# Kernel tuning notes

Hardware: AMD Instinct MI355X
Metric: run time of the kernel (lower is better)

Reference implementation:

```python
import jax, jax.numpy as jnp
import numpy as np

DIM = 128
WINDOW_TOKENS = 64  # window_size**2 = 8*8


def _conv3x3(x, w):
    # x: [B,C,H,W], w: [O,I,3,3], padding=1 (SAME)
    return jax.lax.conv_general_dilated(
        x, w, window_strides=(1, 1), padding='SAME',
        dimension_numbers=('NCHW', 'OIHW', 'NCHW'))


def _pixel_shuffle2(x):
    # torch.nn.PixelShuffle(2): [B, C*4, H, W] -> [B, C, 2H, 2W]
    B, C4, H, W = x.shape
    C = C4 // 4
    x = x.reshape(B, C, 2, 2, H, W)
    x = x.transpose(0, 1, 4, 2, 5, 3)  # [B, C, H, 2, W, 2]
    return x.reshape(B, C, H * 2, W * 2)


def setup_inputs() -> dict:
    key = jax.random.key(0)
    ks = jax.random.split(key, 12)
    B, C = 4, DIM
    f0 = jax.random.normal(ks[0], (B, C, 64, 64), jnp.float32)
    f1 = jax.random.normal(ks[1], (B, C, 128, 128), jnp.float32)
    f2 = jax.random.normal(ks[2], (B, C, 256, 256), jnp.float32)
    s = 0.02
    # Linear weights stored as [in, out] so forward is x @ W
    Wq = jax.random.normal(ks[3], (C, C), jnp.float32) * s
    Wk = jax.random.normal(ks[4], (C, C), jnp.float32) * s
    Wv = jax.random.normal(ks[5], (C, C), jnp.float32) * s
    Wql = jax.random.normal(ks[6], (C, C), jnp.float32) * s
    Wkl = jax.random.normal(ks[7], (C, C), jnp.float32) * s
    Wvl = jax.random.normal(ks[8], (C, C), jnp.float32) * s
    gate_w = jax.random.normal(ks[9], (2 * C, C), jnp.float32) * s
    conv0 = jax.random.normal(ks[10], (4 * C, C, 3, 3), jnp.float32) * s
    conv1 = jax.random.normal(ks[11], (4 * C, C, 3, 3), jnp.float32) * s
    return dict(f0=f0, f1=f1, f2=f2, Wq=Wq, Wk=Wk, Wv=Wv,
                Wql=Wql, Wkl=Wkl, Wvl=Wvl, gate_w=gate_w,
                conv0=conv0, conv1=conv1)


def reference(f0, f1, f2, Wq, Wk, Wv, Wql, Wkl, Wvl, gate_w, conv0, conv1):
    feats = (f0, f1, f2)
    B, C = f0.shape[0], f0.shape[1]
    scale = C ** (-0.5)
    # flatten+concat: [B, N, C]
    toks = [f.reshape(B, C, -1).transpose(0, 2, 1) for f in feats]
    x = jnp.concatenate(toks, axis=1)
    N = x.shape[1]
    wt = WINDOW_TOKENS
    nw = N // wt  # N is divisible by wt for these shapes (no padding)
    windows = x.reshape(B, nw, wt, C)

    # ---- global path (mode='center'): attention over window means ----
    centers = windows.mean(axis=2)  # [B, nw, C]
    Q = centers @ Wq
    K = centers @ Wk
    V = centers @ Wv
    attn = jax.nn.softmax(jnp.einsum('bnc,bmc->bnm', Q, K) * scale, axis=-1)
    y_centers = jnp.einsum('bnm,bmc->bnc', attn, V) * centers
    y_global = jnp.broadcast_to(y_centers[:, :, None, :], (B, nw, wt, C)).reshape(B, N, C)

    # ---- local path: attention within each window (batched over windows) ----
    Ql = windows @ Wql
    Kl = windows @ Wkl
    Vl = windows @ Wvl
    attn_l = jax.nn.softmax(jnp.einsum('bwqc,bwkc->bwqk', Ql, Kl) * scale, axis=-1)
    y_local = (jnp.einsum('bwqk,bwkc->bwqc', attn_l, Vl) * windows).reshape(B, N, C)

    # ---- gated fusion ----
    alpha = jax.nn.sigmoid(jnp.concatenate([y_global, y_local], axis=-1) @ gate_w)
    y = alpha * y_global + (1.0 - alpha) * y_local

    # ---- reshape back to feature maps ----
    maps = []
    start = 0
    for f in feats:
        H, W = f.shape[2], f.shape[3]
        cnt = H * W
        maps.append(y[:, start:start + cnt, :].transpose(0, 2, 1).reshape(B, C, H, W))
        start += cnt
    # ---- inverse wavelet reconstruction (conv3x3 -> pixel shuffle -> add) ----
    outputs = [maps[0]]
    z = maps[0]
    z = _pixel_shuffle2(_conv3x3(z, conv0)) + maps[1]
    outputs.append(z)
    z = _pixel_shuffle2(_conv3x3(z, conv1)) + maps[2]
    outputs.append(z)
    return tuple(outputs)
```

## Files before the change

### kernel.cpp

```cpp
#include <hip/hip_runtime.h>
#include <math.h>

#define WT 64
#define NWIN 1344
#define NP 1408
constexpr float SCALE = 0.088388347648318447f;

#define OUT0 0
#define OUT1 2097152
#define OUT2 10485760

typedef __attribute__((ext_vector_type(8))) short bfrag;
typedef __attribute__((ext_vector_type(8))) _Float16 hfrag;
typedef __attribute__((ext_vector_type(4))) float f32x4;

#define MFMA16 __builtin_amdgcn_mfma_f32_16x16x32_bf16
#define MFMA16H __builtin_amdgcn_mfma_f32_16x16x32_f16

__device__ __forceinline__ unsigned short f2b(float f) {
    union { float f; unsigned u; } v; v.f = f;
    unsigned r = v.u + 0x7fffu + ((v.u >> 16) & 1u);
    return (unsigned short)(r >> 16);
}
__device__ __forceinline__ float b2f(unsigned short u) {
    union { unsigned u; float f; } v; v.u = ((unsigned)u) << 16; return v.f;
}
__device__ __forceinline__ int pack2(float a, float b) {
    return (int)f2b(a) | ((int)f2b(b) << 16);
}

__device__ __forceinline__ bfrag ld256(const char* region, int row, int k) {
    int off = (2 * k) ^ ((row & 7) << 4);
    return *(const bfrag*)(region + row * 256 + off);
}
__device__ __forceinline__ bfrag ld128(const char* region, int row, int k) {
    int off = (2 * k) ^ ((row & 7) << 4);
    return *(const bfrag*)(region + row * 128 + off);
}

__global__ void k_mm(const float* __restrict__ Wq, const float* __restrict__ Wk,
                     float* __restrict__ Mglob) {
    int i = blockIdx.x, j = threadIdx.x;
    float acc = 0.f;
    for (int k = 0; k < 128; ++k) acc += Wq[i * 128 + k] * Wk[j * 128 + k];
    Mglob[i * 128 + j] = acc;
}

__global__ void k_prep(const float* __restrict__ Wql, const float* __restrict__ Wkl,
                       const float* __restrict__ Wvl, const float* __restrict__ gw,
                       unsigned short* __restrict__ MtB,
                       unsigned short* __restrict__ WvltB,
                       unsigned short* __restrict__ G1tB,
                       unsigned short* __restrict__ G0tB) {
    int n = blockIdx.x, k = threadIdx.x;
    if (blockIdx.y == 0) {
        float a = 0.f;
        for (int c = 0; c < 128; ++c) a += Wkl[n * 128 + c] * Wql[k * 128 + c];
        MtB[n * 128 + k] = f2b(a);
    } else if (blockIdx.y == 1) {
        WvltB[n * 128 + k] = f2b(Wvl[k * 128 + n]);
    } else if (blockIdx.y == 2) {
        G1tB[n * 128 + k] = f2b(gw[(128 + k) * 128 + n]);
    } else {
        G0tB[n * 128 + k] = f2b(gw[k * 128 + n]);
    }
}

__global__ __launch_bounds__(256) void k_prep_conv(
    const float* __restrict__ w0, const float* __restrict__ w1,
    _Float16* __restrict__ W0, _Float16* __restrict__ W1) {
    int idx = blockIdx.x * 256 + threadIdx.x;
    const float* w = blockIdx.y ? w1 : w0;
    _Float16* o = blockIdx.y ? W1 : W0;
    int slice = idx >> 14, rem = idx & 16383;
    int oc = rem >> 5, k = rem & 31;
    int ics = slice / 9, tap = slice - ics * 9;
    o[idx] = (_Float16)w[((size_t)oc * 128 + ics * 32 + k) * 9 + tap];
}

__device__ __forceinline__ void window_src(int n0, const float* f0, const float* f1,
                                           const float* f2, const float*& f, int& p0,
                                           int& HW, int& obase) {
    if (n0 < 4096)        { f = f0; p0 = n0;          HW = 4096;  obase = OUT0; }
    else if (n0 < 20480)  { f = f1; p0 = n0 - 4096;   HW = 16384; obase = OUT1; }
    else                  { f = f2; p0 = n0 - 20480;  HW = 65536; obase = OUT2; }
}

__global__ __launch_bounds__(256) void k_centers(
    const float* __restrict__ f0, const float* __restrict__ f1,
    const float* __restrict__ f2, float* __restrict__ ctr,
    unsigned short* __restrict__ ctrb) {
    int w = blockIdx.x, b = blockIdx.y;
    const float* f; int p0, HW, ob;
    window_src(w * WT, f0, f1, f2, f, p0, HW, ob);
    int lane = threadIdx.x & 63, cg = threadIdx.x >> 6;
    for (int c = cg; c < 128; c += 4) {
        float v = f[(b * 128 + c) * HW + p0 + lane];
        #pragma unroll
        for (int off = 32; off; off >>= 1) v += __shfl_xor(v, off);
        if (lane == 0) {
            float mv = v * (1.0f / 64.0f);
            ctr[(b * NWIN + w) * 128 + c] = mv;
            ctrb[(b * NWIN + w) * 128 + c] = f2b(mv);
        }
    }
}

__global__ __launch_bounds__(128) void k_tgvg(
    const float* __restrict__ ctr, const float* __restrict__ Mglob,
    const float* __restrict__ Wv, unsigned short* __restrict__ Tgb,
    unsigned short* __restrict__ Vgt) {
    int n = blockIdx.x, b = blockIdx.y;
    int row = b * NWIN + n;
    int c = threadIdx.x;
    __shared__ __align__(16) float crow[128];
    crow[c] = ctr[row * 128 + c];
    __syncthreads();
    float a1 = 0.f, a2 = 0.f;
    for (int k = 0; k < 128; ++k) {
        float cv = crow[k];
        a1 += cv * Mglob[k * 128 + c];
        a2 += cv * Wv[k * 128 + c];
    }
    Tgb[row * 128 + c] = f2b(a1);
    Vgt[((size_t)b * 128 + c) * NP + n] = f2b(a2);
}

__global__ __launch_bounds__(256, 1) void k_qk(
    const unsigned short* __restrict__ Tgb, const unsigned short* __restrict__ ctrb,
    unsigned short* __restrict__ P) {
    extern __shared__ unsigned short Srow[];
    __shared__ float mxs[32], invs[32];
    int blk = blockIdx.x, b = blockIdx.y;
    int mb = blk * 32;
    int tid = threadIdx.x, wid = tid >> 6, lane = tid & 63;
    int lr = lane & 15, lg = lane >> 4;
    int wm = (wid & 1) * 16, wn = (wid >> 1) * 32;

    const unsigned short* Arow = Tgb + ((size_t)b * NWIN + mb + wm + lr) * 128;
    for (int tile = 0; tile < 21; ++tile) {
        int nb = tile * 64 + wn;
        f32x4 acc[2] = {};
        #pragma unroll
        for (int ks = 0; ks < 4; ++ks) {
            int k = ks * 32 + lg * 8;
            bfrag a = *(const bfrag*)(Arow + k);
            #pragma unroll
            for (int nt = 0; nt < 2; ++nt) {
                bfrag bb = *(const bfrag*)(ctrb + ((size_t)b * NWIN + nb + nt * 16 + lr) * 128 + k);
                acc[nt] = MFMA16(a, bb, acc[nt], 0, 0, 0);
            }
        }
        #pragma unroll
        for (int nt = 0; nt < 2; ++nt) {
            int col = nb + nt * 16 + lr;
            #pragma unroll
            for (int r = 0; r < 4; ++r) {
                int mrow = wm + 4 * lg + r;
                Srow[mrow * 1344 + col] = f2b(acc[nt][r]);
            }
        }
    }
    __syncthreads();
    {
        int row = tid >> 3, sub = tid & 7;
        const unsigned short* sr = Srow + row * 1344;
        float mx = -1e30f;
        for (int c = sub; c < 1344; c += 8) mx = fmaxf(mx, b2f(sr[c]));
        mx = fmaxf(mx, __shfl_xor(mx, 1));
        mx = fmaxf(mx, __shfl_xor(mx, 2));
        mx = fmaxf(mx, __shfl_xor(mx, 4));
        float sum = 0.f;
        for (int c = sub; c < 1344; c += 8) sum += __expf((b2f(sr[c]) - mx) * SCALE);
        sum += __shfl_xor(sum, 1);
        sum += __shfl_xor(sum, 2);
        sum += __shfl_xor(sum, 4);
        if (sub == 0) { mxs[row] = mx; invs[row] = 1.0f / sum; }
    }
    __syncthreads();
    unsigned short* Pb = P + ((size_t)b * NWIN + mb) * NP;
    for (int idx = tid; idx < 32 * (NP / 8); idx += 256) {
        int row = idx / (NP / 8), c8 = idx % (NP / 8);
        float mx = mxs[row], inv = invs[row];
        unsigned short o[8];
        #pragma unroll
        for (int e = 0; e < 8; ++e) {
            int c = c8 * 8 + e;
            float p = (c < 1344) ? __expf((b2f(Srow[row * 1344 + c]) - mx) * SCALE) * inv : 0.f;
            o[e] = f2b(p);
        }
        *(int4*)(Pb + row * NP + c8 * 8) = *(int4*)o;
    }
}

__global__ __launch_bounds__(256) void k_pv(
    const unsigned short* __restrict__ P, const unsigned short* __restrict__ Vgt,
    const float* __restrict__ ctr, float* __restrict__ ycen,
    unsigned short* __restrict__ ycenb) {
    int blk = blockIdx.x, b = blockIdx.y;
    int mb = blk * 32;
    int tid = threadIdx.x, wid = tid >> 6, lane = tid & 63;
    int lr = lane & 15, lg = lane >> 4;
    int cb = wid * 32;
    f32x4 acc[2][2] = {};
    const unsigned short* Pb = P + ((size_t)b * NWIN + mb) * NP;
    const unsigned short* Vb = Vgt + (size_t)b * 128 * NP;
    for (int it = 0; it < 44; ++it) {
        int k = it * 32 + lg * 8;
        bfrag a0 = *(const bfrag*)(Vb + (size_t)(cb + lr) * NP + k);
        bfrag a1 = *(const bfrag*)(Vb + (size_t)(cb + 16 + lr) * NP + k);
        bfrag b0 = *(const bfrag*)(Pb + (size_t)lr * NP + k);
        bfrag b1 = *(const bfrag*)(Pb + (size_t)(16 + lr) * NP + k);
        acc[0][0] = MFMA16(a0, b0, acc[0][0], 0, 0, 0);
        acc[0][1] = MFMA16(a0, b1, acc[0][1], 0, 0, 0);
        acc[1][0] = MFMA16(a1, b0, acc[1][0], 0, 0, 0);
        acc[1][1] = MFMA16(a1, b1, acc[1][1], 0, 0, 0);
    }
    #pragma unroll
    for (int ci = 0; ci < 2; ++ci)
        #pragma unroll
        for (int mj = 0; mj < 2; ++mj) {
            int c0 = cb + ci * 16 + 4 * lg;
            int m = mb + mj * 16 + lr;
            size_t base = ((size_t)b * NWIN + m) * 128 + c0;
            float4 cv = *(const float4*)(ctr + base);
            float4 y;
            y.x = acc[ci][mj][0] * cv.x;
            y.y = acc[ci][mj][1] * cv.y;
            y.z = acc[ci][mj][2] * cv.z;
            y.w = acc[ci][mj][3] * cv.w;
            *(float4*)(ycen + base) = y;
            int2 pv; pv.x = pack2(y.x, y.y); pv.y = pack2(y.z, y.w);
            *(int2*)(ycenb + base) = pv;
        }
}

__global__ __launch_bounds__(256) void k_g0(
    const unsigned short* __restrict__ ycenb, const unsigned short* __restrict__ G0tB,
    float* __restrict__ g0g) {
    int blk = blockIdx.x, b = blockIdx.y;
    int mb = blk * 32;
    int tid = threadIdx.x, wid = tid >> 6, lane = tid & 63;
    int lr = lane & 15, lg = lane >> 4;
    int nb = wid * 32;
    f32x4 acc[2][2] = {};
    const unsigned short* Yb = ycenb + ((size_t)b * NWIN + mb) * 128;
    #pragma unroll
    for (int ks = 0; ks < 4; ++ks) {
        int k = ks * 32 + lg * 8;
        bfrag a0 = *(const bfrag*)(G0tB + (nb + lr) * 128 + k);
        bfrag a1 = *(const bfrag*)(G0tB + (nb + 16 + lr) * 128 + k);
        bfrag b0 = *(const bfrag*)(Yb + lr * 128 + k);
        bfrag b1 = *(const bfrag*)(Yb + (16 + lr) * 128 + k);
        acc[0][0] = MFMA16(a0, b0, acc[0][0], 0, 0, 0);
        acc[0][1] = MFMA16(a0, b1, acc[0][1], 0, 0, 0);
        acc[1][0] = MFMA16(a1, b0, acc[1][0], 0, 0, 0);
        acc[1][1] = MFMA16(a1, b1, acc[1][1], 0, 0, 0);
    }
    #pragma unroll
    for (int ni = 0; ni < 2; ++ni)
        #pragma unroll
        for (int mj = 0; mj < 2; ++mj) {
            int m = mb + mj * 16 + lr;
            int n0 = nb + ni * 16 + 4 * lg;
            #pragma unroll
            for (int r = 0; r < 4; ++r)
                g0g[((size_t)b * NWIN + m) * 128 + n0 + r] = acc[ni][mj][r];
        }
}

#define XB_OFF 0
#define WT_OFF 16384
#define XM_OFF 49152
#define VT_OFF 65536
#define SMEM_SZ 81920

__global__ __launch_bounds__(256, 2) void k_local_mfma(
    const float* __restrict__ f0, const float* __restrict__ f1,
    const float* __restrict__ f2,
    const unsigned short* __restrict__ MtB,
    const unsigned short* __restrict__ WvltB,
    const unsigned short* __restrict__ G1tB,
    const float* __restrict__ g0g, const float* __restrict__ ycen,
    float* __restrict__ out) {
    extern __shared__ char smem[];
    char* Xb = smem + XB_OFF;
    char* Wt = smem + WT_OFF;
    char* XMb = smem + XM_OFF;
    char* Vt = smem + VT_OFF;

    int w = blockIdx.x, b = blockIdx.y;
    const float* f; int p0, HW, obase;
    window_src(w * WT, f0, f1, f2, f, p0, HW, obase);

    int tid = threadIdx.x;
    int wid = tid >> 6, lane = tid & 63;
    int lr = lane & 15, lg = lane >> 4;

    {
        int t0 = tid & 63, cq = tid >> 6;
        const float* src = f + (size_t)(b * 128 + cq * 32) * HW + p0 + t0;
        float xv[32];
        #pragma unroll
        for (int i = 0; i < 32; ++i) xv[i] = src[(size_t)i * HW];
        int4 wreg[8];
        const int4* wsrc = (const int4*)MtB;
        #pragma unroll
        for (int j = 0; j < 8; ++j) wreg[j] = wsrc[j * 256 + tid];
        #pragma unroll
        for (int j = 0; j < 4; ++j) {
            int c0 = cq * 32 + j * 8;
            int4 v;
            v.x = pack2(xv[j * 8 + 0], xv[j * 8 + 1]);
            v.y = pack2(xv[j * 8 + 2], xv[j * 8 + 3]);
            v.z = pack2(xv[j * 8 + 4], xv[j * 8 + 5]);
            v.w = pack2(xv[j * 8 + 6], xv[j * 8 + 7]);
            *(int4*)(Xb + t0 * 256 + ((2 * c0) ^ ((t0 & 7) << 4))) = v;
        }
        #pragma unroll
        for (int j = 0; j < 8; ++j) {
            int ci = j * 256 + tid, n = ci >> 4, pos = ci & 15;
            *(int4*)(Wt + n * 256 + ((pos * 16) ^ ((n & 7) << 4))) = wreg[j];
        }
    }
    __syncthreads();

    int t = 16 * wid + lr;

    {
        f32x4 acc[8] = {};
        #pragma unroll
        for (int ks = 0; ks < 4; ++ks) {
            int k = ks * 32 + lg * 8;
            bfrag xb = ld256(Xb, t, k);
            #pragma unroll
            for (int ct = 0; ct < 8; ++ct) {
                bfrag am = ld256(Wt, 16 * ct + lr, k);
                acc[ct] = MFMA16(am, xb, acc[ct], 0, 0, 0);
            }
        }
        #pragma unroll
        for (int ct = 0; ct < 8; ++ct) {
            int c0 = 16 * ct + 4 * lg;
            int2 v; v.x = pack2(acc[ct][0], acc[ct][1]); v.y = pack2(acc[ct][2], acc[ct][3]);
            *(int2*)(XMb + t * 256 + ((2 * c0) ^ ((t & 7) << 4))) = v;
        }
    }
    __syncthreads();

    {
        int4 wreg[8];
        const int4* wsrc = (const int4*)WvltB;
        #pragma unroll
        for (int j = 0; j < 8; ++j) wreg[j] = wsrc[j * 256 + tid];

        f32x4 s[4] = {};
        #pragma unroll
        for (int ks = 0; ks < 4; ++ks) {
            int k = ks * 32 + lg * 8;
            bfrag bxm = ld256(XMb, t, k);
            #pragma unroll
            for (int ut = 0; ut < 4; ++ut) {
                bfrag ax = ld256(Xb, 16 * ut + lr, k);
                s[ut] = MFMA16(ax, bxm, s[ut], 0, 0, 0);
            }
        }
        float m = -1e30f;
        #pragma unroll
        for (int ut = 0; ut < 4; ++ut)
            #pragma unroll
            for (int r = 0; r < 4; ++r) m = fmaxf(m, s[ut][r]);
        m = fmaxf(m, __shfl_xor(m, 16));
        m = fmaxf(m, __shfl_xor(m, 32));
        float sum = 0.f;
        float e[4][4];
        #pragma unroll
        for (int ut = 0; ut < 4; ++ut)
            #pragma unroll
            for (int r = 0; r < 4; ++r) {
                e[ut][r] = __expf((s[ut][r] - m) * SCALE);
                sum += e[ut][r];
            }
        sum += __shfl_xor(sum, 16);
        sum += __shfl_xor(sum, 32);
        float pinv = 1.0f / sum;
        __syncthreads();
        #pragma unroll
        for (int ut = 0; ut < 4; ++ut) {
            int u0 = 16 * ut + 4 * lg;
            int2 v;
            v.x = pack2(e[ut][0] * pinv, e[ut][1] * pinv);
            v.y = pack2(e[ut][2] * pinv, e[ut][3] * pinv);
            *(int2*)(XMb + t * 128 + ((2 * u0) ^ ((t & 7) << 4))) = v;
        }
        #pragma unroll
        for (int j = 0; j < 8; ++j) {
            int ci = j * 256 + tid, n = ci >> 4, pos = ci & 15;
            *(int4*)(Wt + n * 256 + ((pos * 16) ^ ((n & 7) << 4))) = wreg[j];
        }
    }
    __syncthreads();

    int4 wregG[8];
    {
        const int4* wsrc = (const int4*)G1tB;
        #pragma unroll
        for (int j = 0; j < 8; ++j) wregG[j] = wsrc[j * 256 + tid];

        f32x4 vacc[8] = {};
        #pragma unroll
        for (int ks = 0; ks < 4; ++ks) {
            int k = ks * 32 + lg * 8;
            bfrag ax = ld256(Xb, t, k);
            #pragma unroll
            for (int ct = 0; ct < 8; ++ct) {
                bfrag bw = ld256(Wt, 16 * ct + lr, k);
                vacc[ct] = MFMA16(ax, bw, vacc[ct], 0, 0, 0);
            }
        }
        #pragma unroll
        for (int ct = 0; ct < 8; ++ct) {
            int c = 16 * ct + lr;
            int u0 = 16 * wid + 4 * lg;
            int2 v; v.x = pack2(vacc[ct][0], vacc[ct][1]); v.y = pack2(vacc[ct][2], vacc[ct][3]);
            *(int2*)(Vt + c * 128 + ((2 * u0) ^ ((c & 7) << 4))) = v;
        }
    }
    __syncthreads();

    float yl[8][4];
    float4 yg4[8], g04[8];
    {
        #pragma unroll
        for (int j = 0; j < 8; ++j) {
            int ci = j * 256 + tid, n = ci >> 4, pos = ci & 15;
            *(int4*)(Wt + n * 256 + ((pos * 16) ^ ((n & 7) << 4))) = wregG[j];
        }
        size_t rbase = ((size_t)b * NWIN + w) * 128 + 4 * lg;
        #pragma unroll
        for (int nt = 0; nt < 8; ++nt) {
            yg4[nt] = *(const float4*)(ycen + rbase + 16 * nt);
            g04[nt] = *(const float4*)(g0g + rbase + 16 * nt);
        }
        f32x4 y[8] = {};
        #pragma unroll
        for (int us = 0; us < 2; ++us) {
            int u = us * 32 + lg * 8;
            bfrag bp = ld128(XMb, t, u);
            #pragma unroll
            for (int ct = 0; ct < 8; ++ct) {
                bfrag av = ld128(Vt, 16 * ct + lr, u);
                y[ct] = MFMA16(av, bp, y[ct], 0, 0, 0);
            }
        }
        #pragma unroll
        for (int ct = 0; ct < 8; ++ct) {
            int c0 = 16 * ct + 4 * lg;
            int2 xw = *(const int2*)(Xb + t * 256 + ((2 * c0) ^ ((t & 7) << 4)));
            float x0 = b2f((unsigned short)(xw.x & 0xffff));
            float x1 = b2f((unsigned short)((unsigned)xw.x >> 16));
            float x2 = b2f((unsigned short)(xw.y & 0xffff));
            float x3 = b2f((unsigned short)((unsigned)xw.y >> 16));
            yl[ct][0] = y[ct][0] * x0;
            yl[ct][1] = y[ct][1] * x1;
            yl[ct][2] = y[ct][2] * x2;
            yl[ct][3] = y[ct][3] * x3;
            int2 v; v.x = pack2(yl[ct][0], yl[ct][1]); v.y = pack2(yl[ct][2], yl[ct][3]);
            *(int2*)(Xb + t * 256 + ((2 * c0) ^ ((t & 7) << 4))) = v;
        }
    }
    __syncthreads();

    {
        f32x4 g[8] = {};
        #pragma unroll
        for (int ks = 0; ks < 4; ++ks) {
            int k = ks * 32 + lg * 8;
            bfrag byl = ld256(Xb, t, k);
            #pragma unroll
            for (int nt = 0; nt < 8; ++nt) {
                bfrag ag = ld256(Wt, 16 * nt + lr, k);
                g[nt] = MFMA16(ag, byl, g[nt], 0, 0, 0);
            }
        }
        #pragma unroll
        for (int nt = 0; nt < 8; ++nt) {
            float gv[4] = {g04[nt].x, g04[nt].y, g04[nt].z, g04[nt].w};
            float yv4[4] = {yg4[nt].x, yg4[nt].y, yg4[nt].z, yg4[nt].w};
            #pragma unroll
            for (int r = 0; r < 4; ++r) {
                int c = 16 * nt + 4 * lg + r;
                float a = 1.0f / (1.0f + __expf(-(g[nt][r] + gv[r])));
                float yv = a * yv4[r] + (1.0f - a) * yl[nt][r];
                out[obase + (size_t)(b * 128 + c) * HW + p0 + t] = yv;
            }
        }
    }
}

template <int H, int W>
__global__ __launch_bounds__(256, 2) void k_conv_mfma(
    const float* __restrict__ in, const _Float16* __restrict__ Wcv,
    float* __restrict__ out) {
    constexpr int TXN = W / 32;
    int tile = blockIdx.x;
    int ty = tile / TXN, tx = tile % TXN;
    int y0 = ty * 4, x0 = tx * 32;
    int ob = blockIdx.y * 256;
    int b = blockIdx.z;

    __shared__ __align__(16) char sXs[16384];

    int tid = threadIdx.x;
    int wid = tid >> 6, lane = tid & 63;
    int lr = lane & 15, lg = lane >> 4;

    f32x4 acc[8][4] = {};

    int sy = tid / 34, sx = tid - sy * 34;
    int gy = y0 + sy - 1, gx = x0 + sx - 1;
    bool act = tid < 204;
    bool ok = act && gy >= 0 && gy < H && gx >= 0 && gx < W;
    const float* gp = in + (size_t)b * 128 * H * W + (size_t)gy * W + gx;
    int xswz = (tid >> 3) & 1;

    const _Float16* wbase = Wcv + (size_t)(ob + lr) * 32 + lg * 8;

    hfrag afC[4], afN[4];
    #pragma unroll
    for (int n = 0; n < 4; ++n)
        afC[n] = *(const hfrag*)(wbase + (size_t)(wid * 4 + n) * 512);

    if (act) {
        float xv[32];
        if (ok) {
            #pragma unroll
            for (int ic = 0; ic < 32; ++ic) xv[ic] = gp[(size_t)ic * H * W];
        } else {
            #pragma unroll
            for (int ic = 0; ic < 32; ++ic) xv[ic] = 0.f;
        }
        #pragma unroll
        for (int s = 0; s < 4; ++s) {
            _Float16 hh[8];
            #pragma unroll
            for (int e = 0; e < 8; ++e) hh[e] = (_Float16)xv[s * 8 + e];
            *(int4*)(sXs + tid * 80 + ((s ^ xswz) << 4)) = *(int4*)hh;
        }
    }
    __syncthreads();

    for (int ics = 0; ics < 4; ++ics) {
        if (ics) {
            __syncthreads();
            if (act) {
                float xv[32];
                if (ok) {
                    #pragma unroll
                    for (int ic = 0; ic < 32; ++ic)
                        xv[ic] = gp[(size_t)(ics * 32 + ic) * H * W];
                } else {
                    #pragma unroll
                    for (int ic = 0; ic < 32; ++ic) xv[ic] = 0.f;
                }
                #pragma unroll
                for (int s = 0; s < 4; ++s) {
                    _Float16 hh[8];
                    #pragma unroll
                    for (int e = 0; e < 8; ++e) hh[e] = (_Float16)xv[s * 8 + e];
                    *(int4*)(sXs + tid * 80 + ((s ^ xswz) << 4)) = *(int4*)hh;
                }
            }
            __syncthreads();
        }
        #pragma unroll
        for (int tap = 0; tap < 9; ++tap) {
            int kg = ics * 9 + tap;
            if (tap < 8 || ics < 3) {
                const _Float16* ws = wbase + (size_t)(kg + 1) * 16384;
                #pragma unroll
                for (int n = 0; n < 4; ++n)
                    afN[n] = *(const hfrag*)(ws + (size_t)(wid * 4 + n) * 512);
            }
            int dy = tap / 3, dx = tap - dy * 3;
            hfrag bf[8];
            #pragma unroll
            for (int m = 0; m < 8; ++m) {
                int row = ((m >> 1) + dy) * 34 + (m & 1) * 16 + lr + dx;
                bf[m] = *(const hfrag*)(sXs + row * 80 + ((lg ^ ((row >> 3) & 1)) << 4));
            }
            #pragma unroll
            for (int m = 0; m < 8; ++m)
                #pragma unroll
                for (int n = 0; n < 4; ++n)
                    acc[m][n] = MFMA16H(afC[n], bf[m], acc[m][n], 0, 0, 0);
            #pragma unroll
            for (int n = 0; n < 4; ++n) afC[n] = afN[n];
        }
    }

    float* outb = out + (size_t)b * 128 * 4 * H * W;
    #pragma unroll
    for (int n = 0; n < 4; ++n) {
        int oc0 = ob + (wid * 4 + n) * 16 + lg * 4;
        int c = oc0 >> 2;
        #pragma unroll
        for (int mr = 0; mr < 4; ++mr) {
            int py = y0 + mr;
            #pragma unroll
            for (int i2 = 0; i2 < 2; ++i2) {
                size_t rowb = ((size_t)c * (2 * H) + 2 * py + i2) * (2 * W);
                float2* p0 = (float2*)(outb + rowb + 2 * (x0 + lr));
                float2 v0 = *p0;
                v0.x += acc[2 * mr][n][i2 * 2 + 0];
                v0.y += acc[2 * mr][n][i2 * 2 + 1];
                *p0 = v0;
                float2* p1 = (float2*)(outb + rowb + 2 * (x0 + 16 + lr));
                float2 v1 = *p1;
                v1.x += acc[2 * mr + 1][n][i2 * 2 + 0];
                v1.y += acc[2 * mr + 1][n][i2 * 2 + 1];
                *p1 = v1;
            }
        }
    }
}

extern "C" void kernel_launch(void* const* d_in, const int* in_sizes, int n_in,
                              void* d_out, int out_size, void* d_ws, size_t ws_size,
                              hipStream_t stream) {
    const float* f0 = (const float*)d_in[0];
    const float* f1 = (const float*)d_in[1];
    const float* f2 = (const float*)d_in[2];
    const float* Wq = (const float*)d_in[3];
    const float* Wk = (const float*)d_in[4];
    const float* Wv = (const float*)d_in[5];
    const float* Wql = (const float*)d_in[6];
    const float* Wkl = (const float*)d_in[7];
    const float* Wvl = (const float*)d_in[8];
    const float* gate_w = (const float*)d_in[9];
    const float* conv0 = (const float*)d_in[10];
    const float* conv1 = (const float*)d_in[11];
    float* out = (float*)d_out;
    float* ws = (float*)d_ws;

    float* Mglob = ws;
    float* ctr = Mglob + 16384;
    float* ycen = ctr + 688128;
    float* g0g = ycen + 688128;
    unsigned short* MtB = (unsigned short*)(g0g + 688128);
    unsigned short* WvltB = MtB + 16384;
    unsigned short* G1tB = WvltB + 16384;
    unsigned short* G0tB = G1tB + 16384;
    _Float16* Wcv0 = (_Float16*)(G0tB + 16384);
    _Float16* Wcv1 = Wcv0 + 589824;
    unsigned short* ctrb = (unsigned short*)(Wcv1 + 589824);
    unsigned short* Tgb = ctrb + 688128;
    unsigned short* ycenb = Tgb + 688128;
    unsigned short* Vgt = ycenb + 688128;
    unsigned short* Pg = Vgt + 4 * 128 * NP;

    hipFuncSetAttribute((const void*)k_local_mfma,
                        hipFuncAttributeMaxDynamicSharedMemorySize, SMEM_SZ);
    hipFuncSetAttribute((const void*)k_qk,
                        hipFuncAttributeMaxDynamicSharedMemorySize, 32 * 1344 * 2);

    k_mm<<<dim3(128), 128, 0, stream>>>(Wq, Wk, Mglob);
    k_prep<<<dim3(128, 4), 128, 0, stream>>>(Wql, Wkl, Wvl, gate_w, MtB, WvltB, G1tB, G0tB);
    k_prep_conv<<<dim3(2304, 2), 256, 0, stream>>>(conv0, conv1, Wcv0, Wcv1);
    k_centers<<<dim3(NWIN, 4), 256, 0, stream>>>(f0, f1, f2, ctr, ctrb);
    k_tgvg<<<dim3(NWIN, 4), 128, 0, stream>>>(ctr, Mglob, Wv, Tgb, Vgt);
    k_qk<<<dim3(NWIN / 32, 4), 256, 32 * 1344 * 2, stream>>>(Tgb, ctrb, Pg);
    k_pv<<<dim3(NWIN / 32, 4), 256, 0, stream>>>(Pg, Vgt, ctr, ycen, ycenb);
    k_g0<<<dim3(NWIN / 32, 4), 256, 0, stream>>>(ycenb, G0tB, g0g);
    k_local_mfma<<<dim3(NWIN, 4), 256, SMEM_SZ, stream>>>(
        f0, f1, f2, MtB, WvltB, G1tB, g0g, ycen, out);
    k_conv_mfma<64, 64><<<dim3(32, 2, 4), 256, 0, stream>>>(out + OUT0, Wcv0, out + OUT1);
    k_conv_mfma<128, 128><<<dim3(128, 2, 4), 256, 0, stream>>>(out + OUT1, Wcv1, out + OUT2);
}
```

Baseline: 631.2 us.

## Stream weight fragments from global into registers instead of staging in LDS

The local-window kernel no longer copies the three 128x128 bf16 weight matrices into shared memory. Each wave now loads its MFMA A/B fragments straight from global (L2-resident) memory, double-buffered one k-step ahead in registers. Dropping the weight tile shrinks LDS from 80 KB to 48 KB, and launch bounds are raised to allow 3 blocks per CU. The trade-off is more global/L2 traffic, since every wave reloads the full weights, plus extra register pressure that the higher occupancy target may cause to spill.

```diff
diff --git a/kernel.cpp b/kernel.cpp
--- a/kernel.cpp
+++ b/kernel.cpp
@@ -270,12 +270,11 @@
 }
 
 #define XB_OFF 0
-#define WT_OFF 16384
-#define XM_OFF 49152
-#define VT_OFF 65536
-#define SMEM_SZ 81920
-
-__global__ __launch_bounds__(256, 2) void k_local_mfma(
+#define XM_OFF 16384
+#define VT_OFF 32768
+#define SMEM_SZ 49152
+
+__global__ __launch_bounds__(256, 3) void k_local_mfma(
     const float* __restrict__ f0, const float* __restrict__ f1,
     const float* __restrict__ f2,
     const unsigned short* __restrict__ MtB,
@@ -285,7 +284,6 @@
     float* __restrict__ out) {
     extern __shared__ char smem[];
     char* Xb = smem + XB_OFF;
-    char* Wt = smem + WT_OFF;
     char* XMb = smem + XM_OFF;
     char* Vt = smem + VT_OFF;
 
@@ -296,17 +294,18 @@
     int tid = threadIdx.x;
     int wid = tid >> 6, lane = tid & 63;
     int lr = lane & 15, lg = lane >> 4;
-
+    int k0 = lg * 8;
+
+    bfrag amC[8], amN[8];
+    #pragma unroll
+    for (int ct = 0; ct < 8; ++ct)
+        amC[ct] = *(const bfrag*)(MtB + (16 * ct + lr) * 128 + k0);
     {
         int t0 = tid & 63, cq = tid >> 6;
         const float* src = f + (size_t)(b * 128 + cq * 32) * HW + p0 + t0;
         float xv[32];
         #pragma unroll
         for (int i = 0; i < 32; ++i) xv[i] = src[(size_t)i * HW];
-        int4 wreg[8];
-        const int4* wsrc = (const int4*)MtB;
-        #pragma unroll
-        for (int j = 0; j < 8; ++j) wreg[j] = wsrc[j * 256 + tid];
         #pragma unroll
         for (int j = 0; j < 4; ++j) {
             int c0 = cq * 32 + j * 8;
@@ -317,11 +316,6 @@
             v.w = pack2(xv[j * 8 + 6], xv[j * 8 + 7]);
             *(int4*)(Xb + t0 * 256 + ((2 * c0) ^ ((t0 & 7) << 4))) = v;
         }
-        #pragma unroll
-        for (int j = 0; j < 8; ++j) {
-            int ci = j * 256 + tid, n = ci >> 4, pos = ci & 15;
-            *(int4*)(Wt + n * 256 + ((pos * 16) ^ ((n & 7) << 4))) = wreg[j];
-        }
     }
     __syncthreads();
 
@@ -331,13 +325,18 @@
         f32x4 acc[8] = {};
         #pragma unroll
         for (int ks = 0; ks < 4; ++ks) {
-            int k = ks * 32 + lg * 8;
-            bfrag xb = ld256(Xb, t, k);
-            #pragma unroll
-            for (int ct = 0; ct < 8; ++ct) {
-                bfrag am = ld256(Wt, 16 * ct + lr, k);
-                acc[ct] = MFMA16(am, xb, acc[ct], 0, 0, 0);
-            }
+            if (ks < 3) {
+                int k2 = (ks + 1) * 32 + k0;
+                #pragma unroll
+                for (int ct = 0; ct < 8; ++ct)
+                    amN[ct] = *(const bfrag*)(MtB + (16 * ct + lr) * 128 + k2);
+            }
+            bfrag xb = ld256(Xb, t, ks * 32 + k0);
+            #pragma unroll
+            for (int ct = 0; ct < 8; ++ct)
+                acc[ct] = MFMA16(amC[ct], xb, acc[ct], 0, 0, 0);
+            #pragma unroll
+            for (int ct = 0; ct < 8; ++ct) amC[ct] = amN[ct];
         }
         #pragma unroll
         for (int ct = 0; ct < 8; ++ct) {
@@ -348,16 +347,16 @@
     }
     __syncthreads();
 
+    bfrag wvC[8], wvN[8];
     {
-        int4 wreg[8];
-        const int4* wsrc = (const int4*)WvltB;
-        #pragma unroll
-        for (int j = 0; j < 8; ++j) wreg[j] = wsrc[j * 256 + tid];
+        #pragma unroll
+        for (int ct = 0; ct < 8; ++ct)
+            wvC[ct] = *(const bfrag*)(WvltB + (16 * ct + lr) * 128 + k0);
 
         f32x4 s[4] = {};
         #pragma unroll
         for (int ks = 0; ks < 4; ++ks) {
-            int k = ks * 32 + lg * 8;
+            int k = ks * 32 + k0;
             bfrag bxm = ld256(XMb, t, k);
             #pragma unroll
             for (int ut = 0; ut < 4; ++ut) {
@@ -393,30 +392,25 @@
             v.y = pack2(e[ut][2] * pinv, e[ut][3] * pinv);
             *(int2*)(XMb + t * 128 + ((2 * u0) ^ ((t & 7) << 4))) = v;
         }
-        #pragma unroll
-        for (int j = 0; j < 8; ++j) {
-            int ci = j * 256 + tid, n = ci >> 4, pos = ci & 15;
-            *(int4*)(Wt + n * 256 + ((pos * 16) ^ ((n & 7) << 4))) = wreg[j];
-        }
-    }
-    __syncthreads();
-
-    int4 wregG[8];
+    }
+    __syncthreads();
+
     {
-        const int4* wsrc = (const int4*)G1tB;
-        #pragma unroll
-        for (int j = 0; j < 8; ++j) wregG[j] = wsrc[j * 256 + tid];
-
         f32x4 vacc[8] = {};
         #pragma unroll
         for (int ks = 0; ks < 4; ++ks) {
-            int k = ks * 32 + lg * 8;
-            bfrag ax = ld256(Xb, t, k);
-            #pragma unroll
-            for (int ct = 0; ct < 8; ++ct) {
-                bfrag bw = ld256(Wt, 16 * ct + lr, k);
-                vacc[ct] = MFMA16(ax, bw, vacc[ct], 0, 0, 0);
-            }
+            if (ks < 3) {
+                int k2 = (ks + 1) * 32 + k0;
+                #pragma unroll
+                for (int ct = 0; ct < 8; ++ct)
+                    wvN[ct] = *(const bfrag*)(WvltB + (16 * ct + lr) * 128 + k2);
+            }
+            bfrag ax = ld256(Xb, t, ks * 32 + k0);
+            #pragma unroll
+            for (int ct = 0; ct < 8; ++ct)
+                vacc[ct] = MFMA16(ax, wvC[ct], vacc[ct], 0, 0, 0);
+            #pragma unroll
+            for (int ct = 0; ct < 8; ++ct) wvC[ct] = wvN[ct];
         }
         #pragma unroll
         for (int ct = 0; ct < 8; ++ct) {
@@ -430,12 +424,11 @@
 
     float yl[8][4];
     float4 yg4[8], g04[8];
+    bfrag gC[8], gN[8];
     {
         #pragma unroll
-        for (int j = 0; j < 8; ++j) {
-            int ci = j * 256 + tid, n = ci >> 4, pos = ci & 15;
-            *(int4*)(Wt + n * 256 + ((pos * 16) ^ ((n & 7) << 4))) = wregG[j];
-        }
+        for (int ct = 0; ct < 8; ++ct)
+            gC[ct] = *(const bfrag*)(G1tB + (16 * ct + lr) * 128 + k0);
         size_t rbase = ((size_t)b * NWIN + w) * 128 + 4 * lg;
         #pragma unroll
         for (int nt = 0; nt < 8; ++nt) {
@@ -445,7 +438,7 @@
         f32x4 y[8] = {};
         #pragma unroll
         for (int us = 0; us < 2; ++us) {
-            int u = us * 32 + lg * 8;
+            int u = us * 32 + k0;
             bfrag bp = ld128(XMb, t, u);
             #pragma unroll
             for (int ct = 0; ct < 8; ++ct) {
@@ -475,13 +468,18 @@
         f32x4 g[8] = {};
         #pragma unroll
         for (int ks = 0; ks < 4; ++ks) {
-            int k = ks * 32 + lg * 8;
-            bfrag byl = ld256(Xb, t, k);
-            #pragma unroll
-            for (int nt = 0; nt < 8; ++nt) {
-                bfrag ag = ld256(Wt, 16 * nt + lr, k);
-                g[nt] = MFMA16(ag, byl, g[nt], 0, 0, 0);
-            }
+            if (ks < 3) {
+                int k2 = (ks + 1) * 32 + k0;
+                #pragma unroll
+                for (int nt = 0; nt < 8; ++nt)
+                    gN[nt] = *(const bfrag*)(G1tB + (16 * nt + lr) * 128 + k2);
+            }
+            bfrag byl = ld256(Xb, t, ks * 32 + k0);
+            #pragma unroll
+            for (int nt = 0; nt < 8; ++nt)
+                g[nt] = MFMA16(gC[nt], byl, g[nt], 0, 0, 0);
+            #pragma unroll
+            for (int nt = 0; nt < 8; ++nt) gC[nt] = gN[nt];
         }
         #pragma unroll
         for (int nt = 0; nt < 8; ++nt) {
```

Result: slower. 719.3 us (+14.0%).
